# Kernel tuning notes

Measured on AMD Instinct MI355X. Metric: run time of the kernel, lower is better.

## Reference

```python
import jax, jax.numpy as jnp
import numpy as np
import math

V = 4096; E = 768; H = 12; NL = 4; FFN = 2048; B = 1; L = 2048; HD = E // H
EPS = 1e-5

def _alibi_slopes(n):
    def pow2(m):
        start = 2.0 ** (-2.0 ** (-(math.log2(m) - 3)))
        return [start * start ** i for i in range(m)]
    if math.log2(n).is_integer():
        return np.array(pow2(n), dtype=np.float32)
    c = 2 ** math.floor(math.log2(n))
    s = pow2(c) + pow2(2 * c)[0::2][: n - c]
    return np.array(s, dtype=np.float32)

def _alibi_bias():
    slopes = _alibi_slopes(H)                                   # (H,)
    pos = np.arange(L)
    rel = (pos[None, :] - pos[:, None]).astype(np.float32)      # (L,L), j - i
    return jnp.asarray(slopes[:, None, None] * rel[None])       # (H,L,L)

def _ln(x, g, b):
    m = x.mean(-1, keepdims=True)
    v = ((x - m) ** 2).mean(-1, keepdims=True)
    return (x - m) / jnp.sqrt(v + EPS) * g + b

def setup_inputs():
    key = jax.random.key(0)
    ks = jax.random.split(key, 10)
    s = 0.02
    def rn(k, shape):
        return jax.random.normal(k, shape, dtype=jnp.float32) * s
    embed = rn(ks[0], (V, E)).at[0].set(0.0)   # padding_idx=0 row zeroed
    return dict(
        tokens=jax.random.randint(ks[1], (B, L), 0, V, dtype=jnp.int32),
        attention_mask=jnp.ones((B, L), dtype=jnp.int32),
        embed=embed,
        norm1_g=jnp.ones((NL, E)), norm1_b=jnp.zeros((NL, E)),
        in_w=rn(ks[2], (NL, 3 * E, E)), in_b=jnp.zeros((NL, 3 * E)),
        out_w=rn(ks[3], (NL, E, E)), out_b=jnp.zeros((NL, E)),
        ffn_g=jnp.ones((NL, E)), ffn_bt=jnp.zeros((NL, E)),
        ffn_w1=rn(ks[4], (NL, 2 * FFN, E)), ffn_b1=jnp.zeros((NL, 2 * FFN)),
        ffn_w2=rn(ks[5], (NL, E, FFN)), ffn_b2=jnp.zeros((NL, E)),
        fin_g=jnp.ones((E,)), fin_b=jnp.zeros((E,)),
        mlm_w1=rn(ks[6], (E, E)), mlm_b1=jnp.zeros((E,)),
        mlm_g=jnp.ones((E,)), mlm_bt=jnp.zeros((E,)),
        mlm_w2=rn(ks[7], (V, E)), mlm_b2=jnp.zeros((V,)),
    )

def reference(tokens, attention_mask, embed, norm1_g, norm1_b, in_w, in_b, out_w, out_b,
              ffn_g, ffn_bt, ffn_w1, ffn_b1, ffn_w2, ffn_b2,
              fin_g, fin_b, mlm_w1, mlm_b1, mlm_g, mlm_bt, mlm_w2, mlm_b2):
    x = embed[tokens]                                   # (B,L,E)
    # source adds (attention_mask == 0).float() as a FLOAT key_padding_mask
    # (torch MHA adds float masks directly to scores) -- reproduced faithfully
    key_pad = (attention_mask == 0).astype(x.dtype)     # (B,L)
    bias = _alibi_bias()[None] + key_pad[:, None, None, :]  # (B,H,L,L)
    scale = 1.0 / math.sqrt(HD)
    for i in range(NL):
        # pre-LN multi-head attention with ALiBi bias
        h = _ln(x, norm1_g[i], norm1_b[i])
        qkv = h @ in_w[i].T + in_b[i]                   # (B,L,3E)
        q, k, v = jnp.split(qkv, 3, axis=-1)
        q = q.reshape(B, L, H, HD).transpose(0, 2, 1, 3) * scale
        k = k.reshape(B, L, H, HD).transpose(0, 2, 1, 3)
        v = v.reshape(B, L, H, HD).transpose(0, 2, 1, 3)
        attn = jax.nn.softmax(jnp.einsum('bhqd,bhkd->bhqk', q, k) + bias, axis=-1)
        o = jnp.einsum('bhqk,bhkd->bhqd', attn, v).transpose(0, 2, 1, 3).reshape(B, L, E)
        x = x + (o @ out_w[i].T + out_b[i])
        # GEGLU feed-forward (pre-LN)
        h = _ln(x, ffn_g[i], ffn_bt[i])
        u = h @ ffn_w1[i].T + ffn_b1[i]                 # (B,L,2*FFN)
        a, g = jnp.split(u, 2, axis=-1)
        x = x + ((a * jax.nn.gelu(g, approximate=False)) @ ffn_w2[i].T + ffn_b2[i])
    x = _ln(x, fin_g, fin_b)
    h = jax.nn.gelu(x @ mlm_w1.T + mlm_b1, approximate=False)
    h = _ln(h, mlm_g, mlm_bt)
    return h @ mlm_w2.T + mlm_b2                        # (B,L,V) logits
```

## Files before the change

### kernel.cpp

```cpp
#include <hip/hip_runtime.h>
#include <math.h>
#include <cstdint>

#define L 2048
#define E 768
#define NH 12
#define NL 4
#define FFN 2048
#define VOC 4096
#define LDQKV (3*E)

typedef unsigned short u16;
typedef __bf16 bf16x8 __attribute__((ext_vector_type(8)));
typedef float f32x4 __attribute__((ext_vector_type(4)));

__device__ __forceinline__ float bf2f(u16 u){
  union { unsigned int i; float f; } v; v.i = ((unsigned int)u) << 16; return v.f;
}
__device__ __forceinline__ u16 f2bf(float f){
  union { float fl; unsigned int i; } v; v.fl = f;
  unsigned int r = v.i + 0x7fffu + ((v.i >> 16) & 1u);
  return (u16)(r >> 16);
}
__device__ __forceinline__ float gelu_exact(float x){
  return 0.5f * x * (1.0f + erff(x * 0.70710678118654752f));
}
__device__ __forceinline__ float ldw(const void* p, size_t i, int f32w){
  return f32w ? ((const float*)p)[i] : bf2f(((const u16*)p)[i]);
}

#define MFMA_BF16(a,b,c) __builtin_amdgcn_mfma_f32_16x16x32_bf16(a,b,c,0,0,0)

__device__ __forceinline__ void gload16(const u16* g, const u16* l){
  __builtin_amdgcn_global_load_lds(
      (__attribute__((address_space(1))) void*)(uintptr_t)(const void*)g,
      (__attribute__((address_space(3))) void*)(unsigned int)(uintptr_t)(const void*)l,
      16, 0, 0);
}

__global__ __launch_bounds__(256) void detect_kernel(const u16* __restrict__ emb,
                                                     unsigned int* __restrict__ flag){
  __shared__ int s;
  if (threadIdx.x == 0) s = 0;
  __syncthreads();
  float mx = 0.f;
  for (int i = threadIdx.x; i < 16384; i += 256)
    mx = fmaxf(mx, fabsf(bf2f(emb[2*i])));
  if (mx > 1e4f) s = 1;
  __syncthreads();
  if (threadIdx.x == 0) *flag = (unsigned int)s;
}

__global__ __launch_bounds__(256) void cast4_kernel(const void* __restrict__ src,
                                                    u16* __restrict__ dst, int n4,
                                                    const unsigned int* __restrict__ flag){
  int i4 = blockIdx.x * 256 + threadIdx.x;
  if (i4 >= n4) return;
  size_t i = (size_t)i4 * 4;
  ushort4 o;
  if (*flag){
    const float4 f = ((const float4*)src)[i4];
    o.x = f2bf(f.x); o.y = f2bf(f.y); o.z = f2bf(f.z); o.w = f2bf(f.w);
  } else {
    o = ((const ushort4*)src)[i4];
  }
  *(ushort4*)(dst + i) = o;
}

__global__ __launch_bounds__(256) void padf_kernel(const int* __restrict__ amask,
                                                   float* __restrict__ padf){
  int i = blockIdx.x * 256 + threadIdx.x;
  padf[i] = (amask[i] == 0) ? 1.0f : 0.0f;
}

__global__ __launch_bounds__(256) void embed_kernel(const int* __restrict__ tok,
                                                    const void* __restrict__ emb,
                                                    const unsigned int* __restrict__ flag,
                                                    float* __restrict__ x){
  const int f32w = (int)*flag;
  int idx = blockIdx.x * 256 + threadIdx.x;
  int l = idx / E, e = idx - l * E;
  x[idx] = ldw(emb, (size_t)tok[l] * E + e, f32w);
}

__global__ __launch_bounds__(256) void ln_kernel(const float* __restrict__ x,
                                                 const void* __restrict__ g,
                                                 const void* __restrict__ b,
                                                 size_t goff, size_t boff,
                                                 const unsigned int* __restrict__ flag,
                                                 u16* __restrict__ o){
  const int f32w = (int)*flag;
  const int wave = threadIdx.x >> 6, lane = threadIdx.x & 63;
  const int row = blockIdx.x * 4 + wave;
  const float* xr = x + (size_t)row * E;
  float v[12]; float s = 0.f;
  #pragma unroll
  for (int i = 0; i < 12; i++){ v[i] = xr[lane + i*64]; s += v[i]; }
  #pragma unroll
  for (int off = 32; off > 0; off >>= 1) s += __shfl_xor(s, off);
  const float mean = s * (1.0f / E);
  float vs = 0.f;
  #pragma unroll
  for (int i = 0; i < 12; i++){ float d = v[i] - mean; vs += d * d; }
  #pragma unroll
  for (int off = 32; off > 0; off >>= 1) vs += __shfl_xor(vs, off);
  const float rstd = rsqrtf(vs * (1.0f / E) + 1e-5f);
  u16* orow = o + (size_t)row * E;
  #pragma unroll
  for (int i = 0; i < 12; i++){
    int c = lane + i*64;
    orow[c] = f2bf((v[i] - mean) * rstd * ldw(g, goff + c, f32w) + ldw(b, boff + c, f32w));
  }
}

template<int EPI>
__global__ __launch_bounds__(256)
void gemm_bt(const u16* __restrict__ A, const u16* __restrict__ Bm,
             const void* __restrict__ bias, size_t biasoff,
             const unsigned int* __restrict__ flag,
             u16* __restrict__ outb, float* __restrict__ outf,
             int M, int N, int K){
  __shared__ __align__(16) u16 As[2*128*32];
  __shared__ __align__(16) u16 Bs[2*128*32];
  const int t = threadIdx.x;
  const int lane = t & 63;
  const int col = lane & 15, quad = lane >> 4;
  const int wave = t >> 6;
  const int wr = (wave >> 1) * 64, wc = (wave & 1) * 64;
  const int row0 = blockIdx.y * 128, col0 = blockIdx.x * 128;
  const int f32w = (int)*flag;

  int kb = 0, ke = K;
  if (gridDim.z > 1){ const int kc = K / (int)gridDim.z; kb = blockIdx.z * kc; ke = kb + kc; }

  const int sr = t >> 2;
  const int sc = (t & 3) * 8;
  const u16* Ag = A + (size_t)(row0 + sr) * K + sc;
  const u16* Bg = Bm + (size_t)(col0 + sr) * K + sc;

  f32x4 acc[4][4];
  #pragma unroll
  for (int i = 0; i < 4; i++)
    #pragma unroll
    for (int j = 0; j < 4; j++) acc[i][j] = (f32x4){0.f,0.f,0.f,0.f};

  gload16(Ag + kb,                As + wave*512);
  gload16(Ag + (size_t)64*K + kb, As + wave*512 + 2048);
  gload16(Bg + kb,                Bs + wave*512);
  gload16(Bg + (size_t)64*K + kb, Bs + wave*512 + 2048);

  int p = 0;
  for (int k0 = kb; k0 < ke; k0 += 32, p ^= 1){
    if (k0 + 32 < ke){
      const int nx = (p ^ 1) * 4096;
      gload16(Ag + k0 + 32,                As + nx + wave*512);
      gload16(Ag + (size_t)64*K + k0 + 32, As + nx + wave*512 + 2048);
      gload16(Bg + k0 + 32,                Bs + nx + wave*512);
      gload16(Bg + (size_t)64*K + k0 + 32, Bs + nx + wave*512 + 2048);
      asm volatile("s_waitcnt vmcnt(4)\n\ts_barrier" ::: "memory");
    } else {
      asm volatile("s_waitcnt vmcnt(0)\n\ts_barrier" ::: "memory");
    }
    const u16* Ab = As + p*4096;
    const u16* Bb = Bs + p*4096;
    bf16x8 af[4], bfr[4];
    #pragma unroll
    for (int i = 0; i < 4; i++)
      af[i] = *(const bf16x8*)(Ab + (wr + i*16 + col)*32 + quad*8);
    #pragma unroll
    for (int j = 0; j < 4; j++)
      bfr[j] = *(const bf16x8*)(Bb + (wc + j*16 + col)*32 + quad*8);
    #pragma unroll
    for (int i = 0; i < 4; i++)
      #pragma unroll
      for (int j = 0; j < 4; j++)
        acc[i][j] = MFMA_BF16(af[i], bfr[j], acc[i][j]);
    asm volatile("s_waitcnt lgkmcnt(0)\n\ts_barrier" ::: "memory");
  }

  #pragma unroll
  for (int j = 0; j < 4; j++){
    const int c = col0 + wc + j*16 + col;
    const float bb = (gridDim.z > 1 && blockIdx.z != 0) ? 0.f : ldw(bias, biasoff + c, f32w);
    #pragma unroll
    for (int i = 0; i < 4; i++){
      const int r0 = row0 + wr + i*16 + quad*4;
      #pragma unroll
      for (int rr = 0; rr < 4; rr++){
        const float v = acc[i][j][rr] + bb;
        const size_t idx = (size_t)(r0 + rr) * N + c;
        if (EPI == 0)      outb[idx] = f2bf(v);
        else if (EPI == 1) atomicAdd(&outf[idx], v);
        else if (EPI == 2) outf[idx] = gelu_exact(v);
        else if (EPI == 3) outb[idx] = f2bf(bf2f(outb[idx]) * gelu_exact(v));
        else { if (f32w) outf[idx] = v; else outb[idx] = f2bf(v); }
      }
    }
  }
}

__global__ __launch_bounds__(256)
void vt_kernel(const u16* __restrict__ qkv, u16* __restrict__ Vt){
  const int h = blockIdx.x;
  const int t = threadIdx.x;
  const int d = t & 63;
  const int j0 = blockIdx.y * 32 + (t >> 6) * 8;
  u16 tmp[8];
  #pragma unroll
  for (int jj = 0; jj < 8; jj++)
    tmp[jj] = qkv[(size_t)(j0 + jj) * LDQKV + 2*E + h*64 + d];
  *(ushort4*)(Vt + (size_t)(h*64 + d) * L + j0)     = *(ushort4*)(tmp);
  *(ushort4*)(Vt + (size_t)(h*64 + d) * L + j0 + 4) = *(ushort4*)(tmp + 4);
}

__global__ __launch_bounds__(256)
void attn_mfma(const u16* __restrict__ qkv, const u16* __restrict__ Vt,
               const float* __restrict__ padf, u16* __restrict__ outp){
  const int head = blockIdx.x;
  const int t = threadIdx.x;
  const int wave = t >> 6, lane = t & 63;
  const int col = lane & 15, quad = lane >> 4;
  const int q0 = blockIdx.y * 64 + wave * 16;

  __shared__ __align__(16) u16 Kf[64*64];
  __shared__ __align__(16) u16 Vf[64*64];
  __shared__ __align__(16) u16 Pf[4][16*64];
  u16* P = Pf[wave];

  const float slope = exp2f(head < 8 ? -(float)(head+1) : -0.5f - (float)(head-8));
  const float scale = 0.125f;

  const u16* qrow = qkv + (size_t)(q0 + col) * LDQKV + head*64;
  const bf16x8 qf0 = *(const bf16x8*)(qrow + quad*8);
  const bf16x8 qf1 = *(const bf16x8*)(qrow + 32 + quad*8);

  const u16* kbase  = qkv + E + head*64;
  const u16* vtbase = Vt + (size_t)(head*64) * L;

  const int skey = t >> 2;
  const int stc  = (t & 3) * 16;
  const int kw0  = (((skey >> 4)*8 + (t & 3)*2)*16 + (skey & 15))*8;
  const int kw1  = kw0 + 128;

  float m_i[4] = {-1e30f,-1e30f,-1e30f,-1e30f};
  float l_i[4] = {0.f,0.f,0.f,0.f};
  f32x4 oacc[4];
  #pragma unroll
  for (int nt = 0; nt < 4; nt++) oacc[nt] = (f32x4){0.f,0.f,0.f,0.f};

  const u16* kg = kbase + (size_t)skey * LDQKV + stc;
  const u16* vg = vtbase + (size_t)skey * L + stc;
  bf16x8 kr0 = *(const bf16x8*)(kg), kr1 = *(const bf16x8*)(kg + 8);
  bf16x8 vr0 = *(const bf16x8*)(vg), vr1 = *(const bf16x8*)(vg + 8);

  for (int kt = 0; kt < L; kt += 64){
    *(bf16x8*)(Kf + kw0) = kr0;
    *(bf16x8*)(Kf + kw1) = kr1;
    *(bf16x8*)(Vf + kw0) = vr0;
    *(bf16x8*)(Vf + kw1) = vr1;
    asm volatile("s_waitcnt lgkmcnt(0)\n\ts_barrier" ::: "memory");
    if (kt + 64 < L){
      const u16* kg2 = kbase + (size_t)(kt + 64 + skey) * LDQKV + stc;
      const u16* vg2 = vtbase + (size_t)skey * L + kt + 64 + stc;
      kr0 = *(const bf16x8*)(kg2); kr1 = *(const bf16x8*)(kg2 + 8);
      vr0 = *(const bf16x8*)(vg2); vr1 = *(const bf16x8*)(vg2 + 8);
    }

    f32x4 s[4];
    #pragma unroll
    for (int nt = 0; nt < 4; nt++){
      bf16x8 kf0 = *(const bf16x8*)(Kf + nt*1024 + lane*8);
      bf16x8 kf1 = *(const bf16x8*)(Kf + nt*1024 + 512 + lane*8);
      f32x4 z = (f32x4){0.f,0.f,0.f,0.f};
      z = MFMA_BF16(qf0, kf0, z);
      z = MFMA_BF16(qf1, kf1, z);
      s[nt] = z;
    }
    float padv[4];
    #pragma unroll
    for (int nt = 0; nt < 4; nt++) padv[nt] = padf[kt + nt*16 + col];
    float al[4];
    #pragma unroll
    for (int r = 0; r < 4; r++){
      const float ip = (float)(q0 + quad*4 + r);
      float sv[4]; float mx = -1e30f;
      #pragma unroll
      for (int nt = 0; nt < 4; nt++){
        sv[nt] = s[nt][r] * scale + slope * ((float)(kt + nt*16 + col) - ip) + padv[nt];
        mx = fmaxf(mx, sv[nt]);
      }
      mx = fmaxf(mx, __shfl_xor(mx, 1));
      mx = fmaxf(mx, __shfl_xor(mx, 2));
      mx = fmaxf(mx, __shfl_xor(mx, 4));
      mx = fmaxf(mx, __shfl_xor(mx, 8));
      const float mnew = fmaxf(m_i[r], mx);
      const float a = __expf(m_i[r] - mnew);
      m_i[r] = mnew; al[r] = a;
      float ps = 0.f;
      #pragma unroll
      for (int nt = 0; nt < 4; nt++){
        u16 e = f2bf(__expf(sv[nt] - mnew));
        P[((nt*2 + (col >> 3))*16 + quad*4 + r)*8 + (col & 7)] = e;
        ps += bf2f(e);
      }
      ps += __shfl_xor(ps, 1);
      ps += __shfl_xor(ps, 2);
      ps += __shfl_xor(ps, 4);
      ps += __shfl_xor(ps, 8);
      l_i[r] = l_i[r] * a + ps;
    }
    #pragma unroll
    for (int nt = 0; nt < 4; nt++)
      #pragma unroll
      for (int r = 0; r < 4; r++) oacc[nt][r] *= al[r];

    asm volatile("s_waitcnt lgkmcnt(0)" ::: "memory");
    const bf16x8 pa0 = *(const bf16x8*)(P + lane*8);
    const bf16x8 pa1 = *(const bf16x8*)(P + 512 + lane*8);
    #pragma unroll
    for (int nt = 0; nt < 4; nt++){
      const bf16x8 vb0 = *(const bf16x8*)(Vf + nt*1024 + lane*8);
      const bf16x8 vb1 = *(const bf16x8*)(Vf + nt*1024 + 512 + lane*8);
      oacc[nt] = MFMA_BF16(pa0, vb0, oacc[nt]);
      oacc[nt] = MFMA_BF16(pa1, vb1, oacc[nt]);
    }
    asm volatile("s_waitcnt lgkmcnt(0)\n\ts_barrier" ::: "memory");
  }
  #pragma unroll
  for (int nt = 0; nt < 4; nt++)
    #pragma unroll
    for (int r = 0; r < 4; r++){
      const int row = q0 + quad*4 + r;
      outp[(size_t)row * E + head*64 + nt*16 + col] = f2bf(oacc[nt][r] / l_i[r]);
    }
}

extern "C" void kernel_launch(void* const* d_in, const int* in_sizes, int n_in,
                              void* d_out, int out_size, void* d_ws, size_t ws_size,
                              hipStream_t stream){
  const int* tokens = (const int*)d_in[0];
  const int* amask  = (const int*)d_in[1];

  unsigned int* flag = (unsigned int*)d_ws;
  float* padf = (float*)((char*)d_ws + 256);
  float* x   = padf + L;
  u16* hbuf  = (u16*)(x + (size_t)L*E);
  u16* vtb   = hbuf + (size_t)L*E;
  u16* wc    = vtb + (size_t)NH*64*L;

  const size_t N_INW  = (size_t)NL*3*E*E;
  const size_t N_OUTW = (size_t)NL*E*E;
  const size_t N_FW1  = (size_t)NL*2*FFN*E;
  const size_t N_FW2  = (size_t)NL*E*FFN;
  const size_t N_MW1  = (size_t)E*E;
  const size_t N_MW2  = (size_t)VOC*E;
  u16* in_w  = wc;                 wc += N_INW;
  u16* out_w = wc;                 wc += N_OUTW;
  u16* ffw1  = wc;                 wc += N_FW1;
  u16* ffw2  = wc;                 wc += N_FW2;
  u16* mw1   = wc;                 wc += N_MW1;
  u16* mw2   = wc;                 wc += N_MW2;

  u16* qkvb  = (u16*)d_out;
  u16* attnb = (u16*)d_out + (size_t)L*LDQKV;
  u16* abuf  = (u16*)d_out;
  float* tbuf = (float*)d_out;

  detect_kernel<<<1, 256, 0, stream>>>((const u16*)d_in[2], flag);
  padf_kernel<<<L/256, 256, 0, stream>>>(amask, padf);
  cast4_kernel<<<(int)(N_INW/1024), 256, 0, stream>>>(d_in[5],  in_w,  (int)(N_INW/4),  flag);
  cast4_kernel<<<(int)(N_OUTW/1024),256, 0, stream>>>(d_in[7],  out_w, (int)(N_OUTW/4), flag);
  cast4_kernel<<<(int)(N_FW1/1024), 256, 0, stream>>>(d_in[11], ffw1,  (int)(N_FW1/4),  flag);
  cast4_kernel<<<(int)(N_FW2/1024), 256, 0, stream>>>(d_in[13], ffw2,  (int)(N_FW2/4),  flag);
  cast4_kernel<<<(int)(N_MW1/1024), 256, 0, stream>>>(d_in[17], mw1,   (int)(N_MW1/4),  flag);
  cast4_kernel<<<(int)(N_MW2/1024), 256, 0, stream>>>(d_in[21], mw2,   (int)(N_MW2/4),  flag);

  embed_kernel<<<L*E/256, 256, 0, stream>>>(tokens, d_in[2], flag, x);

  for (int ly = 0; ly < NL; ly++){
    ln_kernel<<<L/4, 256, 0, stream>>>(x, d_in[3], d_in[4],
        (size_t)ly*E, (size_t)ly*E, flag, hbuf);
    gemm_bt<0><<<dim3(3*E/128, L/128), 256, 0, stream>>>(hbuf, in_w + (size_t)ly*3*E*E,
        d_in[6], (size_t)ly*3*E, flag, qkvb, nullptr, L, 3*E, E);
    vt_kernel<<<dim3(NH, L/32), 256, 0, stream>>>(qkvb, vtb);
    attn_mfma<<<dim3(NH, L/64), 256, 0, stream>>>(qkvb, vtb, padf, attnb);
    gemm_bt<1><<<dim3(E/128, L/128, 2), 256, 0, stream>>>(attnb, out_w + (size_t)ly*E*E,
        d_in[8], (size_t)ly*E, flag, nullptr, x, L, E, E);
    ln_kernel<<<L/4, 256, 0, stream>>>(x, d_in[9], d_in[10],
        (size_t)ly*E, (size_t)ly*E, flag, hbuf);
    gemm_bt<0><<<dim3(FFN/128, L/128), 256, 0, stream>>>(hbuf,
        ffw1 + (size_t)ly*2*FFN*E, d_in[12], (size_t)ly*2*FFN, flag,
        abuf, nullptr, L, FFN, E);
    gemm_bt<3><<<dim3(FFN/128, L/128), 256, 0, stream>>>(hbuf,
        ffw1 + (size_t)ly*2*FFN*E + (size_t)FFN*E, d_in[12], (size_t)ly*2*FFN + FFN, flag,
        abuf, nullptr, L, FFN, E);
    gemm_bt<1><<<dim3(E/128, L/128, 2), 256, 0, stream>>>(abuf, ffw2 + (size_t)ly*E*FFN,
        d_in[14], (size_t)ly*E, flag, nullptr, x, L, E, FFN);
  }
  ln_kernel<<<L/4, 256, 0, stream>>>(x, d_in[15], d_in[16], 0, 0, flag, hbuf);
  gemm_bt<2><<<dim3(E/128, L/128), 256, 0, stream>>>(hbuf, mw1,
      d_in[18], 0, flag, nullptr, tbuf, L, E, E);
  ln_kernel<<<L/4, 256, 0, stream>>>(tbuf, d_in[19], d_in[20], 0, 0, flag, hbuf);
  gemm_bt<4><<<dim3(VOC/128, L/128), 256, 0, stream>>>(hbuf, mw2,
      d_in[22], 0, flag, (u16*)d_out, (float*)d_out, L, VOC, E);
}
```

Before: 1.151 ms.

## Split attention keys across two wave groups, transpose scores, precompute ALiBi bias

The attention kernel now launches 512 threads per block. Each half of the block processes one half of the key range, and the two partial softmax states are merged through shared memory at the end. The QK MFMA operands are swapped so each lane holds a single query row, which turns the per-row shuffle reductions into scalar max/sum work with fewer shuffles. A per-head key bias (ALiBi slope times key index plus padding, pre-scaled by log2e) is precomputed so the kernel can use exp2 and packed bf16 conversion. This relies on the row-constant -slope*i term cancelling in softmax. It adds more LDS use, a merge step and a larger block in exchange for more parallelism and less softmax ALU work.

```diff
diff --git a/kernel.cpp b/kernel.cpp
--- a/kernel.cpp
+++ b/kernel.cpp
@@ -9,6 +9,7 @@
 #define FFN 2048
 #define VOC 4096
 #define LDQKV (3*E)
+#define LOG2E 1.4426950408889634f
 
 typedef unsigned short u16;
 typedef __bf16 bf16x8 __attribute__((ext_vector_type(8)));
@@ -67,10 +68,14 @@
   *(ushort4*)(dst + i) = o;
 }
 
-__global__ __launch_bounds__(256) void padf_kernel(const int* __restrict__ amask,
-                                                   float* __restrict__ padf){
+__global__ __launch_bounds__(256) void bias_kernel(const int* __restrict__ amask,
+                                                   float* __restrict__ biasH){
   int i = blockIdx.x * 256 + threadIdx.x;
-  padf[i] = (amask[i] == 0) ? 1.0f : 0.0f;
+  int h = i >> 11;
+  int k = i & (L - 1);
+  float slope = exp2f(h < 8 ? -(float)(h+1) : -0.5f - (float)(h-8));
+  float pad = (amask[k] == 0) ? 1.0f : 0.0f;
+  biasH[i] = (slope * (float)k + pad) * LOG2E;
 }
 
 __global__ __launch_bounds__(256) void embed_kernel(const int* __restrict__ tok,
@@ -213,22 +218,26 @@
   *(ushort4*)(Vt + (size_t)(h*64 + d) * L + j0 + 4) = *(ushort4*)(tmp + 4);
 }
 
-__global__ __launch_bounds__(256)
+__global__ __launch_bounds__(512, 4)
 void attn_mfma(const u16* __restrict__ qkv, const u16* __restrict__ Vt,
-               const float* __restrict__ padf, u16* __restrict__ outp){
+               const float* __restrict__ biasH, u16* __restrict__ outp){
   const int head = blockIdx.x;
   const int t = threadIdx.x;
   const int wave = t >> 6, lane = t & 63;
+  const int grp = wave >> 2, w4 = wave & 3;
   const int col = lane & 15, quad = lane >> 4;
-  const int q0 = blockIdx.y * 64 + wave * 16;
-
-  __shared__ __align__(16) u16 Kf[64*64];
-  __shared__ __align__(16) u16 Vf[64*64];
-  __shared__ __align__(16) u16 Pf[4][16*64];
+  const int q0 = blockIdx.y * 64 + w4 * 16;
+  const int kbeg = grp * (L/2);
+
+  __shared__ __align__(16) u16 Kf[2][64*64];
+  __shared__ __align__(16) u16 Vf[2][64*64];
+  __shared__ __align__(16) u16 Pf[8][16*64];
+  u16* Kg_ = Kf[grp];
+  u16* Vg_ = Vf[grp];
   u16* P = Pf[wave];
 
-  const float slope = exp2f(head < 8 ? -(float)(head+1) : -0.5f - (float)(head-8));
-  const float scale = 0.125f;
+  const float scale2 = 0.125f * LOG2E;
+  const float* bH = biasH + (size_t)head * L + kbeg;
 
   const u16* qrow = qkv + (size_t)(q0 + col) * LDQKV + head*64;
   const bf16x8 qf0 = *(const bf16x8*)(qrow + quad*8);
@@ -237,31 +246,31 @@
   const u16* kbase  = qkv + E + head*64;
   const u16* vtbase = Vt + (size_t)(head*64) * L;
 
-  const int skey = t >> 2;
-  const int stc  = (t & 3) * 16;
-  const int kw0  = (((skey >> 4)*8 + (t & 3)*2)*16 + (skey & 15))*8;
+  const int tg = t & 255;
+  const int skey = tg >> 2;
+  const int stc  = (tg & 3) * 16;
+  const int kw0  = (((skey >> 4)*8 + (tg & 3)*2)*16 + (skey & 15))*8;
   const int kw1  = kw0 + 128;
 
-  float m_i[4] = {-1e30f,-1e30f,-1e30f,-1e30f};
-  float l_i[4] = {0.f,0.f,0.f,0.f};
+  float m_i = -1e30f, l_i = 0.f;
   f32x4 oacc[4];
   #pragma unroll
   for (int nt = 0; nt < 4; nt++) oacc[nt] = (f32x4){0.f,0.f,0.f,0.f};
 
-  const u16* kg = kbase + (size_t)skey * LDQKV + stc;
-  const u16* vg = vtbase + (size_t)skey * L + stc;
+  const u16* kg = kbase + (size_t)(kbeg + skey) * LDQKV + stc;
+  const u16* vg = vtbase + (size_t)skey * L + kbeg + stc;
   bf16x8 kr0 = *(const bf16x8*)(kg), kr1 = *(const bf16x8*)(kg + 8);
   bf16x8 vr0 = *(const bf16x8*)(vg), vr1 = *(const bf16x8*)(vg + 8);
 
-  for (int kt = 0; kt < L; kt += 64){
-    *(bf16x8*)(Kf + kw0) = kr0;
-    *(bf16x8*)(Kf + kw1) = kr1;
-    *(bf16x8*)(Vf + kw0) = vr0;
-    *(bf16x8*)(Vf + kw1) = vr1;
+  for (int kt = 0; kt < L/2; kt += 64){
+    *(bf16x8*)(Kg_ + kw0) = kr0;
+    *(bf16x8*)(Kg_ + kw1) = kr1;
+    *(bf16x8*)(Vg_ + kw0) = vr0;
+    *(bf16x8*)(Vg_ + kw1) = vr1;
     asm volatile("s_waitcnt lgkmcnt(0)\n\ts_barrier" ::: "memory");
-    if (kt + 64 < L){
-      const u16* kg2 = kbase + (size_t)(kt + 64 + skey) * LDQKV + stc;
-      const u16* vg2 = vtbase + (size_t)skey * L + kt + 64 + stc;
+    if (kt + 64 < L/2){
+      const u16* kg2 = kbase + (size_t)(kbeg + kt + 64 + skey) * LDQKV + stc;
+      const u16* vg2 = vtbase + (size_t)skey * L + kbeg + kt + 64 + stc;
       kr0 = *(const bf16x8*)(kg2); kr1 = *(const bf16x8*)(kg2 + 8);
       vr0 = *(const bf16x8*)(vg2); vr1 = *(const bf16x8*)(vg2 + 8);
     }
@@ -269,46 +278,53 @@
     f32x4 s[4];
     #pragma unroll
     for (int nt = 0; nt < 4; nt++){
-      bf16x8 kf0 = *(const bf16x8*)(Kf + nt*1024 + lane*8);
-      bf16x8 kf1 = *(const bf16x8*)(Kf + nt*1024 + 512 + lane*8);
+      const bf16x8 kf0 = *(const bf16x8*)(Kg_ + nt*1024 + lane*8);
+      const bf16x8 kf1 = *(const bf16x8*)(Kg_ + nt*1024 + 512 + lane*8);
       f32x4 z = (f32x4){0.f,0.f,0.f,0.f};
-      z = MFMA_BF16(qf0, kf0, z);
-      z = MFMA_BF16(qf1, kf1, z);
+      z = MFMA_BF16(kf0, qf0, z);
+      z = MFMA_BF16(kf1, qf1, z);
       s[nt] = z;
     }
-    float padv[4];
-    #pragma unroll
-    for (int nt = 0; nt < 4; nt++) padv[nt] = padf[kt + nt*16 + col];
+    float sv[16];
+    #pragma unroll
+    for (int nt = 0; nt < 4; nt++){
+      const float4 bv = *(const float4*)(bH + kt + nt*16 + quad*4);
+      sv[nt*4+0] = fmaf(s[nt][0], scale2, bv.x);
+      sv[nt*4+1] = fmaf(s[nt][1], scale2, bv.y);
+      sv[nt*4+2] = fmaf(s[nt][2], scale2, bv.z);
+      sv[nt*4+3] = fmaf(s[nt][3], scale2, bv.w);
+    }
+    float t8[8];
+    #pragma unroll
+    for (int i = 0; i < 8; i++) t8[i] = fmaxf(sv[i], sv[i+8]);
+    float t4a = fmaxf(t8[0], t8[4]), t4b = fmaxf(t8[1], t8[5]);
+    float t4c = fmaxf(t8[2], t8[6]), t4d = fmaxf(t8[3], t8[7]);
+    float mx = fmaxf(fmaxf(t4a, t4b), fmaxf(t4c, t4d));
+    mx = fmaxf(mx, __shfl_xor(mx, 16));
+    mx = fmaxf(mx, __shfl_xor(mx, 32));
+    const float mnew = fmaxf(m_i, mx);
+    const float a = exp2f(m_i - mnew);
+    m_i = mnew;
+    float ps = 0.f;
+    #pragma unroll
+    for (int nt = 0; nt < 4; nt++){
+      const float e0 = exp2f(sv[nt*4+0] - mnew);
+      const float e1 = exp2f(sv[nt*4+1] - mnew);
+      const float e2 = exp2f(sv[nt*4+2] - mnew);
+      const float e3 = exp2f(sv[nt*4+3] - mnew);
+      unsigned int plo, phi;
+      asm("v_cvt_pk_bf16_f32 %0, %1, %2" : "=v"(plo) : "v"(e0), "v"(e1));
+      asm("v_cvt_pk_bf16_f32 %0, %1, %2" : "=v"(phi) : "v"(e2), "v"(e3));
+      *(uint2*)(P + ((nt*2 + (quad >> 1))*16 + col)*8 + (quad & 1)*4) =
+          make_uint2(plo, phi);
+      ps += (e0 + e1) + (e2 + e3);
+    }
+    ps += __shfl_xor(ps, 16);
+    ps += __shfl_xor(ps, 32);
+    l_i = l_i * a + ps;
     float al[4];
     #pragma unroll
-    for (int r = 0; r < 4; r++){
-      const float ip = (float)(q0 + quad*4 + r);
-      float sv[4]; float mx = -1e30f;
-      #pragma unroll
-      for (int nt = 0; nt < 4; nt++){
-        sv[nt] = s[nt][r] * scale + slope * ((float)(kt + nt*16 + col) - ip) + padv[nt];
-        mx = fmaxf(mx, sv[nt]);
-      }
-      mx = fmaxf(mx, __shfl_xor(mx, 1));
-      mx = fmaxf(mx, __shfl_xor(mx, 2));
-      mx = fmaxf(mx, __shfl_xor(mx, 4));
-      mx = fmaxf(mx, __shfl_xor(mx, 8));
-      const float mnew = fmaxf(m_i[r], mx);
-      const float a = __expf(m_i[r] - mnew);
-      m_i[r] = mnew; al[r] = a;
-      float ps = 0.f;
-      #pragma unroll
-      for (int nt = 0; nt < 4; nt++){
-        u16 e = f2bf(__expf(sv[nt] - mnew));
-        P[((nt*2 + (col >> 3))*16 + quad*4 + r)*8 + (col & 7)] = e;
-        ps += bf2f(e);
-      }
-      ps += __shfl_xor(ps, 1);
-      ps += __shfl_xor(ps, 2);
-      ps += __shfl_xor(ps, 4);
-      ps += __shfl_xor(ps, 8);
-      l_i[r] = l_i[r] * a + ps;
-    }
+    for (int r = 0; r < 4; r++) al[r] = __shfl(a, quad*4 + r);
     #pragma unroll
     for (int nt = 0; nt < 4; nt++)
       #pragma unroll
@@ -319,20 +335,48 @@
     const bf16x8 pa1 = *(const bf16x8*)(P + 512 + lane*8);
     #pragma unroll
     for (int nt = 0; nt < 4; nt++){
-      const bf16x8 vb0 = *(const bf16x8*)(Vf + nt*1024 + lane*8);
-      const bf16x8 vb1 = *(const bf16x8*)(Vf + nt*1024 + 512 + lane*8);
+      const bf16x8 vb0 = *(const bf16x8*)(Vg_ + nt*1024 + lane*8);
+      const bf16x8 vb1 = *(const bf16x8*)(Vg_ + nt*1024 + 512 + lane*8);
       oacc[nt] = MFMA_BF16(pa0, vb0, oacc[nt]);
       oacc[nt] = MFMA_BF16(pa1, vb1, oacc[nt]);
     }
     asm volatile("s_waitcnt lgkmcnt(0)\n\ts_barrier" ::: "memory");
   }
-  #pragma unroll
-  for (int nt = 0; nt < 4; nt++)
+
+  float* cO = (float*)&Kf[0][0];
+  float* cm = (float*)&Vf[0][0];
+  float* cl = cm + 64;
+  if (grp == 1){
+    #pragma unroll
+    for (int nt = 0; nt < 4; nt++)
+      #pragma unroll
+      for (int r = 0; r < 4; r++)
+        cO[(size_t)(w4*64 + lane)*16 + nt*4 + r] = oacc[nt][r];
+    if (quad == 0){ cm[w4*16 + col] = m_i; cl[w4*16 + col] = l_i; }
+  }
+  __syncthreads();
+  if (grp == 0){
+    const float m1 = cm[w4*16 + col], l1 = cl[w4*16 + col];
+    const float M = fmaxf(m_i, m1);
+    const float c0 = exp2f(m_i - M), c1 = exp2f(m1 - M);
+    const float inv = 1.0f / (l_i * c0 + l1 * c1);
+    const float w0 = c0 * inv, w1 = c1 * inv;
+    float s0[4], s1[4];
     #pragma unroll
     for (int r = 0; r < 4; r++){
-      const int row = q0 + quad*4 + r;
-      outp[(size_t)row * E + head*64 + nt*16 + col] = f2bf(oacc[nt][r] / l_i[r]);
-    }
+      s0[r] = __shfl(w0, quad*4 + r);
+      s1[r] = __shfl(w1, quad*4 + r);
+    }
+    #pragma unroll
+    for (int nt = 0; nt < 4; nt++)
+      #pragma unroll
+      for (int r = 0; r < 4; r++){
+        const float o1 = cO[(size_t)(w4*64 + lane)*16 + nt*4 + r];
+        const int row = q0 + quad*4 + r;
+        outp[(size_t)row * E + head*64 + nt*16 + col] =
+            f2bf(oacc[nt][r] * s0[r] + o1 * s1[r]);
+      }
+  }
 }
 
 extern "C" void kernel_launch(void* const* d_in, const int* in_sizes, int n_in,
@@ -342,8 +386,8 @@
   const int* amask  = (const int*)d_in[1];
 
   unsigned int* flag = (unsigned int*)d_ws;
-  float* padf = (float*)((char*)d_ws + 256);
-  float* x   = padf + L;
+  float* biasH = (float*)((char*)d_ws + 256);
+  float* x   = biasH + (size_t)NH*L;
   u16* hbuf  = (u16*)(x + (size_t)L*E);
   u16* vtb   = hbuf + (size_t)L*E;
   u16* wc    = vtb + (size_t)NH*64*L;
@@ -367,7 +411,7 @@
   float* tbuf = (float*)d_out;
 
   detect_kernel<<<1, 256, 0, stream>>>((const u16*)d_in[2], flag);
-  padf_kernel<<<L/256, 256, 0, stream>>>(amask, padf);
+  bias_kernel<<<NH*L/256, 256, 0, stream>>>(amask, biasH);
   cast4_kernel<<<(int)(N_INW/1024), 256, 0, stream>>>(d_in[5],  in_w,  (int)(N_INW/4),  flag);
   cast4_kernel<<<(int)(N_OUTW/1024),256, 0, stream>>>(d_in[7],  out_w, (int)(N_OUTW/4), flag);
   cast4_kernel<<<(int)(N_FW1/1024), 256, 0, stream>>>(d_in[11], ffw1,  (int)(N_FW1/4),  flag);
@@ -383,7 +427,7 @@
     gemm_bt<0><<<dim3(3*E/128, L/128), 256, 0, stream>>>(hbuf, in_w + (size_t)ly*3*E*E,
         d_in[6], (size_t)ly*3*E, flag, qkvb, nullptr, L, 3*E, E);
     vt_kernel<<<dim3(NH, L/32), 256, 0, stream>>>(qkvb, vtb);
-    attn_mfma<<<dim3(NH, L/64), 256, 0, stream>>>(qkvb, vtb, padf, attnb);
+    attn_mfma<<<dim3(NH, L/64), 512, 0, stream>>>(qkvb, vtb, biasH, attnb);
     gemm_bt<1><<<dim3(E/128, L/128, 2), 256, 0, stream>>>(attnb, out_w + (size_t)ly*E*E,
         d_in[8], (size_t)ly*E, flag, nullptr, x, L, E, E);
     ln_kernel<<<L/4, 256, 0, stream>>>(x, d_in[9], d_in[10],
```

Measured after the change: 1.002 ms. -12.9%, faster.
